# Optimization experiments

Hardware: AMD Instinct MI355X
Metric: run time of the kernel (lower is better)

## Reference

```python
import jax, jax.numpy as jnp
import numpy as np

IN_CH = 128
HID = 256   # 2 * out_channels
OUT_CH = 128
N_NODES = 10000
N_EDGES = 640000


def setup_inputs() -> dict:
    key = jax.random.key(0)
    ks = jax.random.split(key, 6)
    x = jax.random.normal(ks[0], (N_NODES, IN_CH), dtype=jnp.float32)
    edge_index = jax.random.randint(ks[1], (2, N_EDGES), 0, N_NODES, dtype=jnp.int64)
    # GCNConv params (glorot-like scale)
    W1 = jax.random.normal(ks[2], (IN_CH, HID), dtype=jnp.float32) / np.sqrt(IN_CH)
    b1 = jnp.zeros((HID,), dtype=jnp.float32)
    W2 = jax.random.normal(ks[3], (HID, OUT_CH), dtype=jnp.float32) / np.sqrt(HID)
    b2 = jnp.zeros((OUT_CH,), dtype=jnp.float32)
    return {"x": x, "edge_index": edge_index, "W1": W1, "b1": b1, "W2": W2, "b2": b2}


def _gcn_norm(edge_index, n_nodes):
    """Add self-loops and compute symmetric GCN normalization per edge."""
    loops = jnp.arange(n_nodes, dtype=edge_index.dtype)
    src = jnp.concatenate([edge_index[0], loops])  # [E+N]
    dst = jnp.concatenate([edge_index[1], loops])
    deg = jax.ops.segment_sum(jnp.ones_like(dst, dtype=jnp.float32), dst,
                              num_segments=n_nodes)
    dinv = jnp.where(deg > 0, jax.lax.rsqrt(deg), 0.0)
    norm = dinv[src] * dinv[dst]  # [E+N]
    return src, dst, norm


def _gcn_layer(x, W, b, src, dst, norm, n_nodes):
    h = x @ W                                  # [N, F_out]
    msg = h[src] * norm[:, None]               # gather + scale, [E+N, F_out]
    agg = jax.ops.segment_sum(msg, dst, num_segments=n_nodes)
    return agg + b


def reference(x, edge_index, W1, b1, W2, b2):
    n = x.shape[0]
    src, dst, norm = _gcn_norm(edge_index, n)
    h = jax.nn.relu(_gcn_layer(x, W1, b1, src, dst, norm, n))
    out = jax.nn.relu(_gcn_layer(h, W2, b2, src, dst, norm, n))
    return out
```

## Files before the change

### kernel.cpp

```cpp
#include <hip/hip_runtime.h>

#define N_FEAT 128
#define HID 256
#define OUT_CH 128

#define NB 256
#define MAXN 10240
#define CH 16
#define CB (NB / CH)

typedef float f32x2 __attribute__((ext_vector_type(2)));

__device__ __forceinline__ unsigned bf16rn(float f) {
    unsigned u = __float_as_uint(f);
    return (u + 0x7fffu + ((u >> 16) & 1u)) >> 16;
}
__device__ __forceinline__ unsigned pack_bf16x2(float lo, float hi) {
    return bf16rn(lo) | (bf16rn(hi) << 16);
}
__device__ __forceinline__ float2 unpack_bf16x2(unsigned u) {
    float2 r;
    r.x = __uint_as_float(u << 16);
    r.y = __uint_as_float(u & 0xffff0000u);
    return r;
}
__device__ __forceinline__ f32x2 unpack_bf16x2v(unsigned u) {
    f32x2 r;
    r.x = __uint_as_float(u << 16);
    r.y = __uint_as_float(u & 0xffff0000u);
    return r;
}


__global__ __launch_bounds__(256)
void hist_kernel(const int* __restrict__ dst, unsigned short* __restrict__ bh,
                 int E, int N, int chunk) {
    __shared__ int hist[MAXN];
    for (int i = threadIdx.x; i < N; i += 256) hist[i] = 0;
    __syncthreads();
    int base = blockIdx.x * chunk;
    int lim = min(chunk, E - base);
    for (int i = threadIdx.x; i < lim; i += 256) {
        int d = dst[base + i];
        if (d >= 0 && d < N) atomicAdd(&hist[d], 1);
    }
    __syncthreads();
    unsigned short* out = bh + (size_t)blockIdx.x * N;
    for (int i = threadIdx.x; i < N; i += 256) out[i] = (unsigned short)hist[i];
}

__global__ __launch_bounds__(256)
void colscan_kernel(const unsigned short* __restrict__ bh,
                    int* __restrict__ ps, int* __restrict__ counts,
                    float* __restrict__ dinv, int N) {
    int j = blockIdx.x * 256 + threadIdx.x;
    if (j >= N) return;
    int run = 0;
    for (int c = 0; c < CH; c++) {
        int s = 0;
        #pragma unroll
        for (int b = c * CB; b < (c + 1) * CB; b++) s += bh[(size_t)b * N + j];
        ps[(size_t)c * N + j] = run;
        run += s;
    }
    counts[j] = run;
    dinv[j] = rsqrtf((float)(run + 1));
}

#define SCAN_T 1024
#define SCAN_MAX_PER 16
__global__ __launch_bounds__(SCAN_T)
void scan_kernel(const int* __restrict__ counts,
                 int* __restrict__ row_start, int n) {
    int tid = threadIdx.x;
    int per = (n + SCAN_T - 1) / SCAN_T;
    int base = tid * per;
    int local[SCAN_MAX_PER];
    int sum = 0;
    for (int j = 0; j < per; j++) {
        int i = base + j;
        int c = (i < n) ? counts[i] : 0;
        local[j] = sum;
        sum += c;
    }
    int lane = tid & 63;
    int wave = tid >> 6;
    int incl = sum;
    #pragma unroll
    for (int off = 1; off < 64; off <<= 1) {
        int t = __shfl_up(incl, off, 64);
        if (lane >= off) incl += t;
    }
    __shared__ int wsum[16];
    __shared__ int woff[16];
    if (lane == 63) wsum[wave] = incl;
    __syncthreads();
    if (wave == 0) {
        int w = (lane < 16) ? wsum[lane] : 0;
        int v = w;
        #pragma unroll
        for (int off = 1; off < 16; off <<= 1) {
            int t = __shfl_up(v, off, 64);
            if (lane >= off) v += t;
        }
        if (lane < 16) woff[lane] = v - w;
    }
    __syncthreads();
    int thread_excl = woff[wave] + (incl - sum);
    for (int j = 0; j < per; j++) {
        int i = base + j;
        if (i < n) row_start[i] = thread_excl + local[j];
    }
    if (tid == SCAN_T - 1) row_start[n] = thread_excl + sum;
}

__global__ __launch_bounds__(256)
void chunkbase_kernel(unsigned short* __restrict__ bh,
                      const int* __restrict__ ps, int N) {
    int j = blockIdx.x * 256 + threadIdx.x;
    if (j >= N) return;
    int c = blockIdx.y;
    int run = ps[(size_t)c * N + j];
    #pragma unroll
    for (int b = c * CB; b < (c + 1) * CB; b++) {
        size_t idx = (size_t)b * N + j;
        int t = bh[idx];
        bh[idx] = (unsigned short)run;
        run += t;
    }
}

__global__ __launch_bounds__(256)
void scat_kernel(const int* __restrict__ src, const int* __restrict__ dst,
                 const unsigned short* __restrict__ bh,
                 const int* __restrict__ row_start,
                 unsigned short* __restrict__ csr_src, int E, int N, int chunk) {
    __shared__ int cur[MAXN];
    const unsigned short* basep = bh + (size_t)blockIdx.x * N;
    for (int i = threadIdx.x; i < N; i += 256)
        cur[i] = row_start[i] + (int)basep[i];
    __syncthreads();
    int base = blockIdx.x * chunk;
    int lim = min(chunk, E - base);
    for (int i = threadIdx.x; i < lim; i += 256) {
        int e = base + i;
        int d = dst[e];
        if (d < 0 || d >= N) continue;
        int pos = atomicAdd(&cur[d], 1);
        if ((unsigned)pos < (unsigned)E) csr_src[pos] = (unsigned short)src[e];
    }
}

__global__ void prescale_kernel(const float* __restrict__ x,
                                const float* __restrict__ dinv,
                                unsigned* __restrict__ xs_b, int total4) {
    int i = blockIdx.x * blockDim.x + threadIdx.x;
    if (i < total4) {
        int row = i >> 5;
        float d = dinv[row];
        float4 v = ((const float4*)x)[i];
        uint2 p;
        p.x = pack_bf16x2(v.x * d, v.y * d);
        p.y = pack_bf16x2(v.z * d, v.w * d);
        ((uint2*)xs_b)[i] = p;
    }
}

template <bool EPILOGUE>
__global__ __launch_bounds__(256)
void agg_kernel(const unsigned* __restrict__ featb,
                const float* __restrict__ dinv,
                const int* __restrict__ row_start,
                const unsigned short* __restrict__ csr_src,
                const float* __restrict__ bias,
                float* __restrict__ out, int N) {
    int wave = threadIdx.x >> 6;
    int n = blockIdx.x * 4 + wave;
    if (n >= N) return;
    int f = threadIdx.x & 63;
    float dn = dinv[n];
    f32x2 acc = unpack_bf16x2v(featb[(size_t)n * 64 + f]);
    int e0 = row_start[n];
    int e1 = row_start[n + 1];
    int e = e0;
    if (e + 8 <= e1) {
        int s_cur[8];
        #pragma unroll
        for (int j = 0; j < 8; j++) s_cur[j] = csr_src[e + j];
        e += 8;
        for (; e + 8 <= e1; e += 8) {
            unsigned w[8];
            #pragma unroll
            for (int j = 0; j < 8; j++) w[j] = featb[(size_t)s_cur[j] * 64 + f];
            int s_nxt[8];
            #pragma unroll
            for (int j = 0; j < 8; j++) s_nxt[j] = csr_src[e + j];
            #pragma unroll
            for (int j = 0; j < 8; j++) acc += unpack_bf16x2v(w[j]);
            #pragma unroll
            for (int j = 0; j < 8; j++) s_cur[j] = s_nxt[j];
        }
        unsigned w[8];
        #pragma unroll
        for (int j = 0; j < 8; j++) w[j] = featb[(size_t)s_cur[j] * 64 + f];
        #pragma unroll
        for (int j = 0; j < 8; j++) acc += unpack_bf16x2v(w[j]);
    }
    for (; e + 4 <= e1; e += 4) {
        int s0 = csr_src[e], s1 = csr_src[e + 1];
        int s2 = csr_src[e + 2], s3 = csr_src[e + 3];
        unsigned w0 = featb[(size_t)s0 * 64 + f];
        unsigned w1 = featb[(size_t)s1 * 64 + f];
        unsigned w2 = featb[(size_t)s2 * 64 + f];
        unsigned w3 = featb[(size_t)s3 * 64 + f];
        acc += unpack_bf16x2v(w0);
        acc += unpack_bf16x2v(w1);
        acc += unpack_bf16x2v(w2);
        acc += unpack_bf16x2v(w3);
    }
    for (; e < e1; ++e)
        acc += unpack_bf16x2v(featb[(size_t)csr_src[e] * 64 + f]);
    acc *= dn;
    float accx = acc.x, accy = acc.y;
    if (EPILOGUE) {
        float2 b = ((const float2*)bias)[f];
        accx = fmaxf(accx + b.x, 0.0f);
        accy = fmaxf(accy + b.y, 0.0f);
    }
    float2 r;
    r.x = accx;
    r.y = accy;
    ((float2*)out)[(size_t)n * 64 + f] = r;
}

template <bool BIAS_RELU, bool RSCALE, bool BF16_OUT>
__global__ __launch_bounds__(256)
void gemm_kernel(const float* __restrict__ A,
                 const float* __restrict__ B,
                 const float* __restrict__ bias,
                 const float* __restrict__ rscale,
                 void* __restrict__ Cv, int M, int N, int K) {
    __shared__ float As[16][68];
    __shared__ float Bs[16][64];
    int tid = threadIdx.x;
    int n0 = blockIdx.x * 64;
    int m0 = blockIdx.y * 64;
    int tx = tid & 15;
    int ty = tid >> 4;
    int ar = tid >> 2;
    int akq = tid & 3;
    int bk = tid >> 4;
    int bnq = tid & 15;
    float acc[4][4] = {};
    for (int k0 = 0; k0 < K; k0 += 16) {
        float4 av = make_float4(0.f, 0.f, 0.f, 0.f);
        if (m0 + ar < M)
            av = *(const float4*)&A[(size_t)(m0 + ar) * K + k0 + akq * 4];
        float4 bv = *(const float4*)&B[(size_t)(k0 + bk) * N + n0 + bnq * 4];
        As[akq * 4 + 0][ar] = av.x;
        As[akq * 4 + 1][ar] = av.y;
        As[akq * 4 + 2][ar] = av.z;
        As[akq * 4 + 3][ar] = av.w;
        *(float4*)&Bs[bk][bnq * 4] = bv;
        __syncthreads();
        #pragma unroll
        for (int k = 0; k < 16; k++) {
            float4 ra = *(const float4*)&As[k][ty * 4];
            float4 rb = *(const float4*)&Bs[k][tx * 4];
            acc[0][0] = fmaf(ra.x, rb.x, acc[0][0]);
            acc[0][1] = fmaf(ra.x, rb.y, acc[0][1]);
            acc[0][2] = fmaf(ra.x, rb.z, acc[0][2]);
            acc[0][3] = fmaf(ra.x, rb.w, acc[0][3]);
            acc[1][0] = fmaf(ra.y, rb.x, acc[1][0]);
            acc[1][1] = fmaf(ra.y, rb.y, acc[1][1]);
            acc[1][2] = fmaf(ra.y, rb.z, acc[1][2]);
            acc[1][3] = fmaf(ra.y, rb.w, acc[1][3]);
            acc[2][0] = fmaf(ra.z, rb.x, acc[2][0]);
            acc[2][1] = fmaf(ra.z, rb.y, acc[2][1]);
            acc[2][2] = fmaf(ra.z, rb.z, acc[2][2]);
            acc[2][3] = fmaf(ra.z, rb.w, acc[2][3]);
            acc[3][0] = fmaf(ra.w, rb.x, acc[3][0]);
            acc[3][1] = fmaf(ra.w, rb.y, acc[3][1]);
            acc[3][2] = fmaf(ra.w, rb.z, acc[3][2]);
            acc[3][3] = fmaf(ra.w, rb.w, acc[3][3]);
        }
        __syncthreads();
    }
    #pragma unroll
    for (int i = 0; i < 4; i++) {
        int m = m0 + ty * 4 + i;
        if (m >= M) continue;
        float rs = RSCALE ? rscale[m] : 1.0f;
        float v[4];
        #pragma unroll
        for (int j = 0; j < 4; j++) {
            v[j] = acc[i][j];
            if (RSCALE) v[j] *= rs;
            if (BIAS_RELU) v[j] = fmaxf(v[j] + bias[n0 + tx * 4 + j], 0.0f);
        }
        if (BF16_OUT) {
            unsigned* Cb = (unsigned*)Cv;
            size_t base = (size_t)m * (N >> 1) + ((n0 + tx * 4) >> 1);
            Cb[base] = pack_bf16x2(v[0], v[1]);
            Cb[base + 1] = pack_bf16x2(v[2], v[3]);
        } else {
            float* C = (float*)Cv;
            #pragma unroll
            for (int j = 0; j < 4; j++)
                C[(size_t)m * N + n0 + tx * 4 + j] = v[j];
        }
    }
}


static inline size_t align512(size_t x) { return (x + 511) & ~(size_t)511; }

extern "C" void kernel_launch(void* const* d_in, const int* in_sizes, int n_in,
                              void* d_out, int out_size, void* d_ws, size_t ws_size,
                              hipStream_t stream) {
    const float* x = (const float*)d_in[0];
    const int* ei = (const int*)d_in[1];
    const float* W1 = (const float*)d_in[2];
    const float* b1 = (const float*)d_in[3];
    const float* W2 = (const float*)d_in[4];
    const float* b2 = (const float*)d_in[5];
    float* out = (float*)d_out;

    const int N = in_sizes[0] / N_FEAT;
    const int E = in_sizes[1] / 2;
    const int* src = ei;
    const int* dst = ei + E;

    char* ws = (char*)d_ws;
    size_t off = 0;
    float* dinv = (float*)(ws + off);    off += align512((size_t)N * 4);
    int* counts = (int*)(ws + off);      off += align512((size_t)N * 4);
    int* row_start = (int*)(ws + off);   off += align512((size_t)(N + 1) * 4);
    unsigned short* csr_src = (unsigned short*)(ws + off);
    off += align512((size_t)E * 2);
    unsigned* xs_b = (unsigned*)(ws + off); off += align512((size_t)N * 64 * 4);
    float* h = (float*)(ws + off);       off += align512((size_t)N * HID * 4);
    unsigned* t_b = (unsigned*)(ws + off); off += align512((size_t)N * 64 * 4);
    int* ps = (int*)(ws + off);          off += align512((size_t)CH * N * 4);
    unsigned short* bh = (unsigned short*)(ws + off);
    off += align512((size_t)NB * N * 2);
    (void)ws_size;
    float* agg1 = out;
    const int chunk = (E + NB - 1) / NB;
    const int NJ = (N + 255) / 256;

    hist_kernel<<<NB, 256, 0, stream>>>(dst, bh, E, N, chunk);
    colscan_kernel<<<NJ, 256, 0, stream>>>(bh, ps, counts, dinv, N);
    scan_kernel<<<1, SCAN_T, 0, stream>>>(counts, row_start, N);
    chunkbase_kernel<<<dim3(NJ, CH), 256, 0, stream>>>(bh, ps, N);
    scat_kernel<<<NB, 256, 0, stream>>>(src, dst, bh, row_start, csr_src, E, N, chunk);

    {
        int total4 = N * N_FEAT / 4;
        prescale_kernel<<<(total4 + 255) / 256, 256, 0, stream>>>(x, dinv, xs_b, total4);
    }

    agg_kernel<false><<<(N + 3) / 4, 256, 0, stream>>>(xs_b, dinv, row_start, csr_src,
                                                       nullptr, agg1, N);

    {
        dim3 grid(HID / 64, (N + 63) / 64);
        gemm_kernel<true, false, false><<<grid, 256, 0, stream>>>(
            agg1, W1, b1, nullptr, h, N, HID, N_FEAT);
    }

    {
        dim3 grid(OUT_CH / 64, (N + 63) / 64);
        gemm_kernel<false, true, true><<<grid, 256, 0, stream>>>(
            h, W2, nullptr, dinv, t_b, N, OUT_CH, HID);
    }

    agg_kernel<true><<<(N + 3) / 4, 256, 0, stream>>>(t_b, dinv, row_start, csr_src,
                                                      b2, out, N);
}
```

Measured before the change: 176.4 us.

## Split wave into two half-waves gathering alternate edges with 8-byte loads

The aggregation kernel now assigns each half of a 64-lane wave to alternate edges, so each lane loads 8 bytes (four bf16 features) per neighbor instead of 4. Source indices are read two at a time as packed 32-bit words, and the halves are combined with a cross-lane shuffle before scaling and an optional bias+ReLU. The aim is wider memory transactions and fewer index loads per edge. The cost is extra alignment and tail handling, shuffle reductions, and half the wave idling on the odd-edge and tail paths.

```diff
diff --git a/kernel.cpp b/kernel.cpp
--- a/kernel.cpp
+++ b/kernel.cpp
@@ -177,60 +177,93 @@
     int wave = threadIdx.x >> 6;
     int n = blockIdx.x * 4 + wave;
     if (n >= N) return;
-    int f = threadIdx.x & 63;
-    float dn = dinv[n];
-    f32x2 acc = unpack_bf16x2v(featb[(size_t)n * 64 + f]);
-    int e0 = row_start[n];
-    int e1 = row_start[n + 1];
+    int l = threadIdx.x & 63;
+    int half = l >> 5;
+    int fl = l & 31;
+    const uint2* feat2 = (const uint2*)featb;
+    f32x2 a01 = {0.f, 0.f}, a23 = {0.f, 0.f};
+    if (half == 0) {
+        uint2 s = feat2[(size_t)n * 32 + fl];
+        a01 = unpack_bf16x2v(s.x);
+        a23 = unpack_bf16x2v(s.y);
+    }
+    int e0 = row_start[n], e1 = row_start[n + 1];
     int e = e0;
+    if ((e & 1) && e < e1) {
+        if (half == 0) {
+            uint2 w = feat2[(size_t)csr_src[e] * 32 + fl];
+            a01 += unpack_bf16x2v(w.x);
+            a23 += unpack_bf16x2v(w.y);
+        }
+        e++;
+    }
+    const unsigned* cs2 = (const unsigned*)csr_src;
     if (e + 8 <= e1) {
-        int s_cur[8];
-        #pragma unroll
-        for (int j = 0; j < 8; j++) s_cur[j] = csr_src[e + j];
+        unsigned p_cur[4];
+        #pragma unroll
+        for (int j = 0; j < 4; j++) p_cur[j] = cs2[(e >> 1) + j];
         e += 8;
         for (; e + 8 <= e1; e += 8) {
-            unsigned w[8];
+            uint2 w[4];
             #pragma unroll
-            for (int j = 0; j < 8; j++) w[j] = featb[(size_t)s_cur[j] * 64 + f];
-            int s_nxt[8];
+            for (int j = 0; j < 4; j++) {
+                int s = half ? (int)(p_cur[j] >> 16) : (int)(p_cur[j] & 0xffffu);
+                w[j] = feat2[(size_t)s * 32 + fl];
+            }
+            unsigned p_nxt[4];
             #pragma unroll
-            for (int j = 0; j < 8; j++) s_nxt[j] = csr_src[e + j];
+            for (int j = 0; j < 4; j++) p_nxt[j] = cs2[(e >> 1) + j];
             #pragma unroll
-            for (int j = 0; j < 8; j++) acc += unpack_bf16x2v(w[j]);
+            for (int j = 0; j < 4; j++) {
+                a01 += unpack_bf16x2v(w[j].x);
+                a23 += unpack_bf16x2v(w[j].y);
+            }
             #pragma unroll
-            for (int j = 0; j < 8; j++) s_cur[j] = s_nxt[j];
-        }
-        unsigned w[8];
-        #pragma unroll
-        for (int j = 0; j < 8; j++) w[j] = featb[(size_t)s_cur[j] * 64 + f];
-        #pragma unroll
-        for (int j = 0; j < 8; j++) acc += unpack_bf16x2v(w[j]);
-    }
-    for (; e + 4 <= e1; e += 4) {
-        int s0 = csr_src[e], s1 = csr_src[e + 1];
-        int s2 = csr_src[e + 2], s3 = csr_src[e + 3];
-        unsigned w0 = featb[(size_t)s0 * 64 + f];
-        unsigned w1 = featb[(size_t)s1 * 64 + f];
-        unsigned w2 = featb[(size_t)s2 * 64 + f];
-        unsigned w3 = featb[(size_t)s3 * 64 + f];
-        acc += unpack_bf16x2v(w0);
-        acc += unpack_bf16x2v(w1);
-        acc += unpack_bf16x2v(w2);
-        acc += unpack_bf16x2v(w3);
-    }
-    for (; e < e1; ++e)
-        acc += unpack_bf16x2v(featb[(size_t)csr_src[e] * 64 + f]);
-    acc *= dn;
-    float accx = acc.x, accy = acc.y;
+            for (int j = 0; j < 4; j++) p_cur[j] = p_nxt[j];
+        }
+        uint2 w[4];
+        #pragma unroll
+        for (int j = 0; j < 4; j++) {
+            int s = half ? (int)(p_cur[j] >> 16) : (int)(p_cur[j] & 0xffffu);
+            w[j] = feat2[(size_t)s * 32 + fl];
+        }
+        #pragma unroll
+        for (int j = 0; j < 4; j++) {
+            a01 += unpack_bf16x2v(w[j].x);
+            a23 += unpack_bf16x2v(w[j].y);
+        }
+    }
+    for (; e + 2 <= e1; e += 2) {
+        unsigned p = cs2[e >> 1];
+        int s = half ? (int)(p >> 16) : (int)(p & 0xffffu);
+        uint2 w = feat2[(size_t)s * 32 + fl];
+        a01 += unpack_bf16x2v(w.x);
+        a23 += unpack_bf16x2v(w.y);
+    }
+    if (e < e1 && half == 0) {
+        uint2 w = feat2[(size_t)csr_src[e] * 32 + fl];
+        a01 += unpack_bf16x2v(w.x);
+        a23 += unpack_bf16x2v(w.y);
+    }
+    a01.x += __shfl_xor(a01.x, 32, 64);
+    a01.y += __shfl_xor(a01.y, 32, 64);
+    a23.x += __shfl_xor(a23.x, 32, 64);
+    a23.y += __shfl_xor(a23.y, 32, 64);
+    float dn = dinv[n];
+    a01 *= dn;
+    a23 *= dn;
     if (EPILOGUE) {
-        float2 b = ((const float2*)bias)[f];
-        accx = fmaxf(accx + b.x, 0.0f);
-        accy = fmaxf(accy + b.y, 0.0f);
-    }
-    float2 r;
-    r.x = accx;
-    r.y = accy;
-    ((float2*)out)[(size_t)n * 64 + f] = r;
+        float4 b = ((const float4*)bias)[fl];
+        a01.x = fmaxf(a01.x + b.x, 0.0f);
+        a01.y = fmaxf(a01.y + b.y, 0.0f);
+        a23.x = fmaxf(a23.x + b.z, 0.0f);
+        a23.y = fmaxf(a23.y + b.w, 0.0f);
+    }
+    if (half == 0) {
+        float4 r;
+        r.x = a01.x; r.y = a01.y; r.z = a23.x; r.w = a23.y;
+        ((float4*)out)[(size_t)n * 32 + fl] = r;
+    }
 }
 
 template <bool BIAS_RELU, bool RSCALE, bool BF16_OUT>
```

Result: slower. 180.0 us (+2.0%).
